# Performance work log

Measured on AMD Instinct MI355X. Metric: run time of the kernel, lower is better.

The kernel has to match this reference:

```python
import jax, jax.numpy as jnp
import numpy as np


def setup_inputs() -> dict:
    B, Lq, Lk, D, F, H = 2, 2048, 2048, 128, 128, 8
    key = jax.random.key(0)
    ks = jax.random.split(key, 8)
    X_Q = jax.random.normal(ks[0], (B, Lq, D), dtype=jnp.float32)
    X_K = jax.random.normal(ks[1], (B, Lk, D), dtype=jnp.float32)
    X_V = jax.random.normal(ks[2], (B, Lk, F), dtype=jnp.float32)
    mask = jax.random.randint(ks[3], (B, 1, Lq, Lk), 0, 2, dtype=jnp.int32)
    # xavier_normal for [H, D, D]: std = sqrt(2/(D+D))
    W_Q = jax.random.normal(ks[4], (H, D, D), dtype=jnp.float32) * np.sqrt(2.0 / (D + D))
    W_K = jax.random.normal(ks[5], (H, D, D), dtype=jnp.float32) * np.sqrt(2.0 / (D + D))
    W_V = jax.random.normal(ks[6], (H, F, F), dtype=jnp.float32) * np.sqrt(2.0 / (F + F))
    O = jax.random.normal(ks[7], (F * H, F), dtype=jnp.float32) * np.sqrt(2.0 / (F * H + F))
    return {"X_Q": X_Q, "X_K": X_K, "X_V": X_V, "mask": mask,
            "W_Q": W_Q, "W_K": W_K, "W_V": W_V, "O": O}


def reference(X_Q, X_K, X_V, mask, W_Q, W_K, W_V, O):
    B, Lq, D = X_Q.shape
    H = W_Q.shape[0]
    F = W_V.shape[1]
    # torch.einsum with repeated in-operand index ('hdd') takes the diagonal
    dq = jnp.diagonal(W_Q, axis1=1, axis2=2)  # [H, D]
    dk = jnp.diagonal(W_K, axis1=1, axis2=2)  # [H, D]
    dv = jnp.diagonal(W_V, axis1=1, axis2=2)  # [H, F]
    g = dq * dk                               # fused per-head QK diagonal scale [H, D]
    scale = 1.0 / jnp.sqrt(jnp.asarray(D, dtype=X_Q.dtype))
    scores = jnp.einsum('bqd,hd,bkd->bhqk', X_Q, g, X_K) * scale  # [B,H,Lq,Lk]
    scores = jnp.where(mask == 0, jnp.asarray(-jnp.inf, scores.dtype), scores)
    A = jax.nn.softmax(scores, axis=-1)
    # O_h = A @ (diag(dv_h) scaled V)
    Oh = jnp.einsum('bhqk,hf,bkf->bhqf', A, dv, X_V)  # [B,H,Lq,F]
    Oh = Oh.transpose(0, 2, 1, 3).reshape(B, Lq, H * F)
    return jnp.einsum('bqx,xf->bqf', Oh, O)
```

## Files before the change

### kernel.cpp

```cpp
#include <hip/hip_runtime.h>

typedef __bf16 bf16;
typedef __bf16 bf16x4 __attribute__((ext_vector_type(4)));
typedef __bf16 bf16x8 __attribute__((ext_vector_type(8)));
typedef float f32x4 __attribute__((ext_vector_type(4)));
typedef unsigned int u32;
typedef unsigned long long u64;

#define B_ 2
#define H_ 8
#define L_ 2048
#define D_ 128
#define F_ 128
#define QT 64
#define KT 64
#define NKT (L_ / KT)

#define WS_KB 0u
#define WS_VT (1u << 20)
#define WS_MB (2u << 20)

#define SMEM_BYTES 74752
#define SP_OFF 65536
#define SP_STRIDE 72
#define SOH_STRIDE 136
#define SO2_STRIDE 136

__device__ __forceinline__ void dma16(const void* g, void* l) {
    __builtin_amdgcn_global_load_lds(
        (const __attribute__((address_space(1))) u32*)g,
        (__attribute__((address_space(3))) u32*)l, 16, 0, 0);
}

__global__ __launch_bounds__(256) void prep_k(const float* __restrict__ XK, bf16* __restrict__ Kb) {
    int gid = blockIdx.x * 256 + threadIdx.x;
    int row = gid >> 4;
    int j   = gid & 15;
    const float* src = XK + (size_t)row * 128 + j * 8;
    float4 v0 = *(const float4*)src;
    float4 v1 = *(const float4*)(src + 4);
    bf16x8 w;
    w[0] = (bf16)v0.x; w[1] = (bf16)v0.y; w[2] = (bf16)v0.z; w[3] = (bf16)v0.w;
    w[4] = (bf16)v1.x; w[5] = (bf16)v1.y; w[6] = (bf16)v1.z; w[7] = (bf16)v1.w;
    int jp = j ^ (row & 15);
    *(bf16x8*)(Kb + (size_t)row * 128 + jp * 8) = w;
}

__global__ __launch_bounds__(256) void prep_v(const float* __restrict__ XV, bf16* __restrict__ Vtb) {
    __shared__ bf16 sT[64 * 128];
    int tile = blockIdx.x;
    int b = tile >> 5, kt = tile & 31;
    int k0 = kt * 64;
    int tid = threadIdx.x;
    int f4 = (tid & 31) * 4, kr = tid >> 5;
    #pragma unroll
    for (int i = 0; i < 8; ++i) {
        int k = kr + i * 8;
        float4 v = *(const float4*)(XV + (size_t)(b * L_ + k0 + k) * F_ + f4);
        bf16x4 w;
        w[0] = (bf16)v.x; w[1] = (bf16)v.y; w[2] = (bf16)v.z; w[3] = (bf16)v.w;
        *(bf16x4*)(sT + k * 128 + f4) = w;
    }
    __syncthreads();
    bf16* out = Vtb + (size_t)tile * (128 * 64);
    #pragma unroll
    for (int i = 0; i < 4; ++i) {
        int cid = tid * 4 + i;
        int f = cid >> 3, j = cid & 7;
        bf16x8 w;
        #pragma unroll
        for (int jj = 0; jj < 8; ++jj) w[jj] = sT[(j * 8 + jj) * 128 + f];
        *(bf16x8*)(out + f * 64 + (j ^ (f & 7)) * 8) = w;
    }
}

__global__ __launch_bounds__(256) void prep_mask(const int* __restrict__ mask, u64* __restrict__ bits) {
    size_t gid = (size_t)blockIdx.x * 256 + threadIdx.x;
    int m = mask[gid];
    u64 bal = __ballot(m != 0);
    if ((threadIdx.x & 63) == 0) bits[gid >> 6] = bal;
}

__global__ __launch_bounds__(256, 2)
void attn_fused_kernel(const float* __restrict__ XQ, const bf16* __restrict__ Kb,
                       const bf16* __restrict__ Vtb, const u64* __restrict__ bits,
                       const float* __restrict__ WQ, const float* __restrict__ WK,
                       const float* __restrict__ WV, const float* __restrict__ Om,
                       float* __restrict__ out)
{
    __shared__ __align__(16) char smem[SMEM_BYTES];
    __shared__ __align__(16) float g_s[128];

    bf16* sK0 = (bf16*)smem;
    bf16* sK1 = (bf16*)(smem + 16384);
    bf16* sV0 = (bf16*)(smem + 32768);
    bf16* sV1 = (bf16*)(smem + 49152);
    bf16* sP  = (bf16*)(smem + SP_OFF);
    bf16* sOh  = (bf16*)smem;
    bf16* sO2t = (bf16*)(smem + 17408);

    const int tid  = threadIdx.x;
    const int wave = tid >> 6;
    const int lane = tid & 63;
    const int c    = lane & 15;
    const int quad = lane >> 4;
    const int qt = blockIdx.x, h = blockIdx.y, b = blockIdx.z;
    const int q0 = qt * QT;
    const int fv  = tid & 127;
    const int grp = tid >> 7;

    if (tid < 128) {
        float wq = WQ[(h * D_ + tid) * D_ + tid];
        float wk = WK[(h * D_ + tid) * D_ + tid];
        g_s[tid] = wq * wk * 0.08838834764831845f;
    }
    __syncthreads();

    const char* gKbase = (const char*)Kb + (size_t)(b * L_) * 256;
    const char* gVbase = (const char*)Vtb + (size_t)(b * NKT) * 16384;

    #pragma unroll
    for (int i = 0; i < 4; ++i) dma16(gKbase + i * 4096 + tid * 16, (char*)sK0 + i * 4096 + tid * 16);
    #pragma unroll
    for (int i = 0; i < 4; ++i) dma16(gVbase + i * 4096 + tid * 16, (char*)sV0 + i * 4096 + tid * 16);

    bf16x8 qfrag[4];
    {
        const float* qrow = XQ + (size_t)(b * L_ + q0 + wave * 16 + c) * D_;
        #pragma unroll
        for (int kc = 0; kc < 4; ++kc) {
            int d0 = kc * 32 + quad * 8;
            float4 v0 = *(const float4*)(qrow + d0);
            float4 v1 = *(const float4*)(qrow + d0 + 4);
            float4 g0 = *(const float4*)(g_s + d0);
            float4 g1 = *(const float4*)(g_s + d0 + 4);
            bf16x8 w;
            w[0] = (bf16)(v0.x * g0.x); w[1] = (bf16)(v0.y * g0.y);
            w[2] = (bf16)(v0.z * g0.z); w[3] = (bf16)(v0.w * g0.w);
            w[4] = (bf16)(v1.x * g1.x); w[5] = (bf16)(v1.y * g1.y);
            w[6] = (bf16)(v1.z * g1.z); w[7] = (bf16)(v1.w * g1.w);
            qfrag[kc] = w;
        }
    }

    const int qrow0 = q0 + wave * 16 + quad * 4;
    const u64* mbase0 = bits + (size_t)(b * L_ + qrow0) * NKT;

    f32x4 oacc[8];
    #pragma unroll
    for (int i = 0; i < 8; ++i)
        #pragma unroll
        for (int r = 0; r < 4; ++r) oacc[i][r] = 0.f;
    float lsum[4] = {0.f, 0.f, 0.f, 0.f};

    #pragma unroll 2
    for (int kt = 0; kt < NKT; ++kt) {
        bf16* sK  = (kt & 1) ? sK1 : sK0;
        bf16* sV  = (kt & 1) ? sV1 : sV0;
        bf16* sKn = (kt & 1) ? sK0 : sK1;
        bf16* sVn = (kt & 1) ? sV0 : sV1;

        asm volatile("s_barrier" ::: "memory");

        u64 mb[4];
        const u64* mbase = mbase0 + kt;
        if (kt + 1 < NKT) {
            const char* gk = gKbase + (size_t)(kt + 1) * 16384;
            const char* gv = gVbase + (size_t)(kt + 1) * 16384;
            #pragma unroll
            for (int i = 0; i < 4; ++i) dma16(gk + i * 4096 + tid * 16, (char*)sKn + i * 4096 + tid * 16);
            #pragma unroll
            for (int i = 0; i < 4; ++i) dma16(gv + i * 4096 + tid * 16, (char*)sVn + i * 4096 + tid * 16);
            #pragma unroll
            for (int r = 0; r < 4; ++r) mb[r] = mbase[(size_t)r * NKT];
            asm volatile("s_waitcnt vmcnt(12)" ::: "memory");
        } else {
            #pragma unroll
            for (int r = 0; r < 4; ++r) mb[r] = mbase[(size_t)r * NKT];
            asm volatile("s_waitcnt vmcnt(4)" ::: "memory");
        }
        asm volatile("s_barrier" ::: "memory");

        f32x4 sacc[4];
        #pragma unroll
        for (int nt = 0; nt < 4; ++nt)
            #pragma unroll
            for (int r = 0; r < 4; ++r) sacc[nt][r] = 0.f;

        #pragma unroll
        for (int nt = 0; nt < 4; ++nt) {
            const bf16* krow = sK + (nt * 16 + c) * 128;
            #pragma unroll
            for (int kc = 0; kc < 4; ++kc) {
                bf16x8 bfrag = *(const bf16x8*)(krow + (((kc * 4 + quad) ^ c) * 8));
                sacc[nt] = __builtin_amdgcn_mfma_f32_16x16x32_bf16(qfrag[kc], bfrag, sacc[nt], 0, 0, 0);
            }
        }

        #pragma unroll
        for (int nt = 0; nt < 4; ++nt) {
            #pragma unroll
            for (int r = 0; r < 4; ++r) {
                float p = ((mb[r] >> (nt * 16 + c)) & 1ull) ? __expf(sacc[nt][r]) : 0.f;
                lsum[r] += p;
                sP[(wave * 16 + quad * 4 + r) * SP_STRIDE + nt * 16 + c] = (bf16)p;
            }
        }
        asm volatile("s_waitcnt lgkmcnt(0)" ::: "memory");

        bf16x8 pfrag[2];
        const bf16* prow = sP + (wave * 16 + c) * SP_STRIDE;
        #pragma unroll
        for (int kc = 0; kc < 2; ++kc)
            pfrag[kc] = *(const bf16x8*)(prow + kc * 32 + quad * 8);

        #pragma unroll
        for (int nt = 0; nt < 8; ++nt) {
            const bf16* vrow = sV + (nt * 16 + c) * 64;
            #pragma unroll
            for (int kc = 0; kc < 2; ++kc) {
                bf16x8 bfrag = *(const bf16x8*)(vrow + (((kc * 4 + quad) ^ (c & 7)) * 8));
                oacc[nt] = __builtin_amdgcn_mfma_f32_16x16x32_bf16(pfrag[kc], bfrag, oacc[nt], 0, 0, 0);
            }
        }
    }

    #pragma unroll
    for (int r = 0; r < 4; ++r) {
        float v = lsum[r];
        v += __shfl_xor(v, 1); v += __shfl_xor(v, 2);
        v += __shfl_xor(v, 4); v += __shfl_xor(v, 8);
        lsum[r] = 1.0f / v;
    }

    __syncthreads();

    if (tid < 128)
        g_s[tid] = WV[(h * F_ + tid) * F_ + tid];

    #pragma unroll
    for (int nt = 0; nt < 8; ++nt)
        #pragma unroll
        for (int r = 0; r < 4; ++r) {
            float v = oacc[nt][r] * lsum[r];
            sOh[(wave * 16 + quad * 4 + r) * SOH_STRIDE + nt * 16 + c] = (bf16)v;
        }
    __syncthreads();

    #pragma unroll
    for (int i = 0; i < 16; ++i) {
        int fp4 = grp * 64 + i * 4;
        bf16x4 w;
        #pragma unroll
        for (int j = 0; j < 4; ++j) {
            int x = fp4 + j;
            w[j] = (bf16)(Om[(h * F_ + x) * F_ + fv] * g_s[x]);
        }
        *(bf16x4*)(sO2t + fv * SO2_STRIDE + fp4) = w;
    }
    __syncthreads();

    bf16x8 afr[4];
    const bf16* ohrow = sOh + (wave * 16 + c) * SOH_STRIDE;
    #pragma unroll
    for (int kc = 0; kc < 4; ++kc)
        afr[kc] = *(const bf16x8*)(ohrow + kc * 32 + quad * 8);

    #pragma unroll
    for (int nt = 0; nt < 8; ++nt) {
        f32x4 pacc;
        #pragma unroll
        for (int r = 0; r < 4; ++r) pacc[r] = 0.f;
        const bf16* orow = sO2t + (nt * 16 + c) * SO2_STRIDE;
        #pragma unroll
        for (int kc = 0; kc < 4; ++kc) {
            bf16x8 bfrag = *(const bf16x8*)(orow + kc * 32 + quad * 8);
            pacc = __builtin_amdgcn_mfma_f32_16x16x32_bf16(afr[kc], bfrag, pacc, 0, 0, 0);
        }
        #pragma unroll
        for (int r = 0; r < 4; ++r) {
            int qg = q0 + wave * 16 + quad * 4 + r;
            atomicAdd(out + ((size_t)(b * L_ + qg) * F_ + nt * 16 + c), pacc[r]);
        }
    }
}

extern "C" void kernel_launch(void* const* d_in, const int* in_sizes, int n_in,
                              void* d_out, int out_size, void* d_ws, size_t ws_size,
                              hipStream_t stream) {
    const float* XQ   = (const float*)d_in[0];
    const float* XK   = (const float*)d_in[1];
    const float* XV   = (const float*)d_in[2];
    const int*   mask = (const int*)d_in[3];
    const float* WQ   = (const float*)d_in[4];
    const float* WK   = (const float*)d_in[5];
    const float* WV   = (const float*)d_in[6];
    const float* Om   = (const float*)d_in[7];
    float* out = (float*)d_out;

    char* ws = (char*)d_ws;
    bf16* Kb   = (bf16*)(ws + WS_KB);
    bf16* Vtb  = (bf16*)(ws + WS_VT);
    u64*  bits = (u64*)(ws + WS_MB);

    prep_k<<<256, 256, 0, stream>>>(XK, Kb);
    prep_v<<<B_ * NKT, 256, 0, stream>>>(XV, Vtb);
    prep_mask<<<(B_ * L_ * L_) / 256, 256, 0, stream>>>(mask, bits);
    hipMemsetAsync(out, 0, (size_t)out_size * sizeof(float), stream);

    dim3 grid(L_ / QT, H_, B_);
    attn_fused_kernel<<<grid, 256, 0, stream>>>(XQ, Kb, Vtb, bits, WQ, WK, WV, Om, out);
}
```

Measured before the change: 170.4 us.

## Split attention work by key rows per wave and fuse prep kernels

Merges the three preprocessing kernels (mask bit-packing, K conversion, V transpose) into one launch. The mask pass now has each wave handle four ballots, and V is transposed straight from global memory without a shared-memory stage. In the attention loop, each wave now computes the transposed score tile for its own 16 keys against all 64 queries. The PV product is then split as a 2x2 query-by-feature grid across the four waves, which needs an extra barrier per key tile and a cross-wave row-sum reduction through shared memory. Mask words are loaded per query row before the prefetch issue, and the added register pressure from qfrag[4][4] may hurt occupancy.

```diff
diff --git a/kernel.cpp b/kernel.cpp
--- a/kernel.cpp
+++ b/kernel.cpp
@@ -20,9 +20,10 @@
 #define WS_VT (1u << 20)
 #define WS_MB (2u << 20)
 
-#define SMEM_BYTES 74752
+#define SMEM_BYTES 75776
 #define SP_OFF 65536
 #define SP_STRIDE 72
+#define LWS_OFF 74752
 #define SOH_STRIDE 136
 #define SO2_STRIDE 136
 
@@ -32,53 +33,48 @@
         (__attribute__((address_space(3))) u32*)l, 16, 0, 0);
 }
 
-__global__ __launch_bounds__(256) void prep_k(const float* __restrict__ XK, bf16* __restrict__ Kb) {
-    int gid = blockIdx.x * 256 + threadIdx.x;
-    int row = gid >> 4;
-    int j   = gid & 15;
-    const float* src = XK + (size_t)row * 128 + j * 8;
-    float4 v0 = *(const float4*)src;
-    float4 v1 = *(const float4*)(src + 4);
-    bf16x8 w;
-    w[0] = (bf16)v0.x; w[1] = (bf16)v0.y; w[2] = (bf16)v0.z; w[3] = (bf16)v0.w;
-    w[4] = (bf16)v1.x; w[5] = (bf16)v1.y; w[6] = (bf16)v1.z; w[7] = (bf16)v1.w;
-    int jp = j ^ (row & 15);
-    *(bf16x8*)(Kb + (size_t)row * 128 + jp * 8) = w;
-}
-
-__global__ __launch_bounds__(256) void prep_v(const float* __restrict__ XV, bf16* __restrict__ Vtb) {
-    __shared__ bf16 sT[64 * 128];
-    int tile = blockIdx.x;
-    int b = tile >> 5, kt = tile & 31;
-    int k0 = kt * 64;
-    int tid = threadIdx.x;
-    int f4 = (tid & 31) * 4, kr = tid >> 5;
-    #pragma unroll
-    for (int i = 0; i < 8; ++i) {
-        int k = kr + i * 8;
-        float4 v = *(const float4*)(XV + (size_t)(b * L_ + k0 + k) * F_ + f4);
-        bf16x4 w;
-        w[0] = (bf16)v.x; w[1] = (bf16)v.y; w[2] = (bf16)v.z; w[3] = (bf16)v.w;
-        *(bf16x4*)(sT + k * 128 + f4) = w;
-    }
-    __syncthreads();
-    bf16* out = Vtb + (size_t)tile * (128 * 64);
-    #pragma unroll
-    for (int i = 0; i < 4; ++i) {
-        int cid = tid * 4 + i;
-        int f = cid >> 3, j = cid & 7;
+__global__ __launch_bounds__(256)
+void prep_all(const float* __restrict__ XK, const float* __restrict__ XV,
+              const int* __restrict__ mask, bf16* __restrict__ Kb,
+              bf16* __restrict__ Vtb, u64* __restrict__ bits)
+{
+    const int bid = blockIdx.x;
+    const int tid = threadIdx.x;
+    if (bid < 8192) {
+        int wv = bid * 4 + (tid >> 6);
+        int lane = tid & 63;
+        size_t base = (size_t)wv * 256;
+        #pragma unroll
+        for (int s = 0; s < 4; ++s) {
+            int m = mask[base + s * 64 + lane];
+            u64 bal = __ballot(m != 0);
+            if (lane == 0) bits[(size_t)wv * 4 + s] = bal;
+        }
+    } else if (bid < 8448) {
+        int gid = (bid - 8192) * 256 + tid;
+        int row = gid >> 4;
+        int j   = gid & 15;
+        const float* src = XK + (size_t)row * 128 + j * 8;
+        float4 v0 = *(const float4*)src;
+        float4 v1 = *(const float4*)(src + 4);
         bf16x8 w;
-        #pragma unroll
-        for (int jj = 0; jj < 8; ++jj) w[jj] = sT[(j * 8 + jj) * 128 + f];
-        *(bf16x8*)(out + f * 64 + (j ^ (f & 7)) * 8) = w;
-    }
-}
-
-__global__ __launch_bounds__(256) void prep_mask(const int* __restrict__ mask, u64* __restrict__ bits) {
-    size_t gid = (size_t)blockIdx.x * 256 + threadIdx.x;
-    int m = mask[gid];
-    u64 bal = __ballot(m != 0);
-    if ((threadIdx.x & 63) == 0) bits[gid >> 6] = bal;
+        w[0] = (bf16)v0.x; w[1] = (bf16)v0.y; w[2] = (bf16)v0.z; w[3] = (bf16)v0.w;
+        w[4] = (bf16)v1.x; w[5] = (bf16)v1.y; w[6] = (bf16)v1.z; w[7] = (bf16)v1.w;
+        int jp = j ^ (row & 15);
+        *(bf16x8*)(Kb + (size_t)row * 128 + jp * 8) = w;
+    } else {
+        int idx  = bid - 8448;
+        int tile = idx >> 2;
+        int fq   = idx & 3;
+        int f    = fq * 32 + (tid & 31);
+        int j    = tid >> 5;
+        int bb   = tile >> 5, kt = tile & 31;
+        const float* src = XV + ((size_t)(bb * L_ + kt * 64 + j * 8)) * F_ + f;
+        bf16x8 w;
+        #pragma unroll
+        for (int jj = 0; jj < 8; ++jj) w[jj] = (bf16)src[(size_t)jj * F_];
+        *(bf16x8*)(Vtb + (size_t)tile * 8192 + f * 64 + ((j ^ (f & 7)) * 8)) = w;
+    }
 }
 
 __global__ __launch_bounds__(256, 2)
@@ -96,6 +92,7 @@
     bf16* sV0 = (bf16*)(smem + 32768);
     bf16* sV1 = (bf16*)(smem + 49152);
     bf16* sP  = (bf16*)(smem + SP_OFF);
+    float* lws = (float*)(smem + LWS_OFF);
     bf16* sOh  = (bf16*)smem;
     bf16* sO2t = (bf16*)(smem + 17408);
 
@@ -106,6 +103,8 @@
     const int quad = lane >> 4;
     const int qt = blockIdx.x, h = blockIdx.y, b = blockIdx.z;
     const int q0 = qt * QT;
+    const int mh = wave >> 1;
+    const int fh = wave & 1;
     const int fv  = tid & 127;
     const int grp = tid >> 7;
 
@@ -124,9 +123,10 @@
     #pragma unroll
     for (int i = 0; i < 4; ++i) dma16(gVbase + i * 4096 + tid * 16, (char*)sV0 + i * 4096 + tid * 16);
 
-    bf16x8 qfrag[4];
-    {
-        const float* qrow = XQ + (size_t)(b * L_ + q0 + wave * 16 + c) * D_;
+    bf16x8 qfrag[4][4];
+    #pragma unroll
+    for (int mt = 0; mt < 4; ++mt) {
+        const float* qrow = XQ + (size_t)(b * L_ + q0 + mt * 16 + c) * D_;
         #pragma unroll
         for (int kc = 0; kc < 4; ++kc) {
             int d0 = kc * 32 + quad * 8;
@@ -139,19 +139,20 @@
             w[2] = (bf16)(v0.z * g0.z); w[3] = (bf16)(v0.w * g0.w);
             w[4] = (bf16)(v1.x * g1.x); w[5] = (bf16)(v1.y * g1.y);
             w[6] = (bf16)(v1.z * g1.z); w[7] = (bf16)(v1.w * g1.w);
-            qfrag[kc] = w;
-        }
-    }
-
-    const int qrow0 = q0 + wave * 16 + quad * 4;
-    const u64* mbase0 = bits + (size_t)(b * L_ + qrow0) * NKT;
-
-    f32x4 oacc[8];
-    #pragma unroll
-    for (int i = 0; i < 8; ++i)
-        #pragma unroll
-        for (int r = 0; r < 4; ++r) oacc[i][r] = 0.f;
+            qfrag[mt][kc] = w;
+        }
+    }
+
+    f32x4 oacc[2][4];
+    #pragma unroll
+    for (int mi = 0; mi < 2; ++mi)
+        #pragma unroll
+        for (int fi = 0; fi < 4; ++fi)
+            #pragma unroll
+            for (int r = 0; r < 4; ++r) oacc[mi][fi][r] = 0.f;
     float lsum[4] = {0.f, 0.f, 0.f, 0.f};
+
+    const int shift = wave * 16 + quad * 4;
 
     #pragma unroll 2
     for (int kt = 0; kt < NKT; ++kt) {
@@ -163,7 +164,10 @@
         asm volatile("s_barrier" ::: "memory");
 
         u64 mb[4];
-        const u64* mbase = mbase0 + kt;
+        #pragma unroll
+        for (int mt = 0; mt < 4; ++mt)
+            mb[mt] = bits[(size_t)(b * L_ + q0 + mt * 16 + c) * NKT + kt];
+
         if (kt + 1 < NKT) {
             const char* gk = gKbase + (size_t)(kt + 1) * 16384;
             const char* gv = gVbase + (size_t)(kt + 1) * 16384;
@@ -171,80 +175,88 @@
             for (int i = 0; i < 4; ++i) dma16(gk + i * 4096 + tid * 16, (char*)sKn + i * 4096 + tid * 16);
             #pragma unroll
             for (int i = 0; i < 4; ++i) dma16(gv + i * 4096 + tid * 16, (char*)sVn + i * 4096 + tid * 16);
-            #pragma unroll
-            for (int r = 0; r < 4; ++r) mb[r] = mbase[(size_t)r * NKT];
             asm volatile("s_waitcnt vmcnt(12)" ::: "memory");
         } else {
-            #pragma unroll
-            for (int r = 0; r < 4; ++r) mb[r] = mbase[(size_t)r * NKT];
             asm volatile("s_waitcnt vmcnt(4)" ::: "memory");
         }
         asm volatile("s_barrier" ::: "memory");
 
-        f32x4 sacc[4];
-        #pragma unroll
-        for (int nt = 0; nt < 4; ++nt)
-            #pragma unroll
-            for (int r = 0; r < 4; ++r) sacc[nt][r] = 0.f;
-
-        #pragma unroll
-        for (int nt = 0; nt < 4; ++nt) {
-            const bf16* krow = sK + (nt * 16 + c) * 128;
-            #pragma unroll
-            for (int kc = 0; kc < 4; ++kc) {
-                bf16x8 bfrag = *(const bf16x8*)(krow + (((kc * 4 + quad) ^ c) * 8));
-                sacc[nt] = __builtin_amdgcn_mfma_f32_16x16x32_bf16(qfrag[kc], bfrag, sacc[nt], 0, 0, 0);
+        f32x4 tacc[4];
+        #pragma unroll
+        for (int mt = 0; mt < 4; ++mt)
+            #pragma unroll
+            for (int r = 0; r < 4; ++r) tacc[mt][r] = 0.f;
+
+        const bf16* krow = sK + (wave * 16 + c) * 128;
+        #pragma unroll
+        for (int kc = 0; kc < 4; ++kc) {
+            bf16x8 kfrag = *(const bf16x8*)(krow + (((kc * 4 + quad) ^ c) * 8));
+            #pragma unroll
+            for (int mt = 0; mt < 4; ++mt)
+                tacc[mt] = __builtin_amdgcn_mfma_f32_16x16x32_bf16(kfrag, qfrag[mt][kc], tacc[mt], 0, 0, 0);
+        }
+
+        #pragma unroll
+        for (int mt = 0; mt < 4; ++mt) {
+            bf16x4 pw;
+            #pragma unroll
+            for (int r = 0; r < 4; ++r) {
+                float p = ((mb[mt] >> (shift + r)) & 1ull) ? __expf(tacc[mt][r]) : 0.f;
+                lsum[mt] += p;
+                pw[r] = (bf16)p;
             }
-        }
-
-        #pragma unroll
-        for (int nt = 0; nt < 4; ++nt) {
-            #pragma unroll
-            for (int r = 0; r < 4; ++r) {
-                float p = ((mb[r] >> (nt * 16 + c)) & 1ull) ? __expf(sacc[nt][r]) : 0.f;
-                lsum[r] += p;
-                sP[(wave * 16 + quad * 4 + r) * SP_STRIDE + nt * 16 + c] = (bf16)p;
+            *(bf16x4*)(sP + (mt * 16 + c) * SP_STRIDE + shift) = pw;
+        }
+        asm volatile("s_waitcnt lgkmcnt(0)" ::: "memory");
+        asm volatile("s_barrier" ::: "memory");
+
+        #pragma unroll
+        for (int kc = 0; kc < 2; ++kc) {
+            bf16x8 pfrag[2];
+            #pragma unroll
+            for (int mi = 0; mi < 2; ++mi)
+                pfrag[mi] = *(const bf16x8*)(sP + ((2 * mh + mi) * 16 + c) * SP_STRIDE + kc * 32 + quad * 8);
+            #pragma unroll
+            for (int fi = 0; fi < 4; ++fi) {
+                const bf16* vrow = sV + ((fh * 4 + fi) * 16 + c) * 64;
+                bf16x8 vfrag = *(const bf16x8*)(vrow + (((kc * 4 + quad) ^ (c & 7)) * 8));
+                #pragma unroll
+                for (int mi = 0; mi < 2; ++mi)
+                    oacc[mi][fi] = __builtin_amdgcn_mfma_f32_16x16x32_bf16(pfrag[mi], vfrag, oacc[mi][fi], 0, 0, 0);
             }
         }
-        asm volatile("s_waitcnt lgkmcnt(0)" ::: "memory");
-
-        bf16x8 pfrag[2];
-        const bf16* prow = sP + (wave * 16 + c) * SP_STRIDE;
-        #pragma unroll
-        for (int kc = 0; kc < 2; ++kc)
-            pfrag[kc] = *(const bf16x8*)(prow + kc * 32 + quad * 8);
-
-        #pragma unroll
-        for (int nt = 0; nt < 8; ++nt) {
-            const bf16* vrow = sV + (nt * 16 + c) * 64;
-            #pragma unroll
-            for (int kc = 0; kc < 2; ++kc) {
-                bf16x8 bfrag = *(const bf16x8*)(vrow + (((kc * 4 + quad) ^ (c & 7)) * 8));
-                oacc[nt] = __builtin_amdgcn_mfma_f32_16x16x32_bf16(pfrag[kc], bfrag, oacc[nt], 0, 0, 0);
-            }
-        }
-    }
-
-    #pragma unroll
-    for (int r = 0; r < 4; ++r) {
-        float v = lsum[r];
-        v += __shfl_xor(v, 1); v += __shfl_xor(v, 2);
-        v += __shfl_xor(v, 4); v += __shfl_xor(v, 8);
-        lsum[r] = 1.0f / v;
-    }
-
+    }
+
+    #pragma unroll
+    for (int mt = 0; mt < 4; ++mt) {
+        float v = lsum[mt];
+        v += __shfl_xor(v, 16); v += __shfl_xor(v, 32);
+        if (lane < 16) lws[wave * 64 + mt * 16 + lane] = v;
+    }
     __syncthreads();
 
     if (tid < 128)
         g_s[tid] = WV[(h * F_ + tid) * F_ + tid];
 
-    #pragma unroll
-    for (int nt = 0; nt < 8; ++nt)
+    float linv[2][4];
+    #pragma unroll
+    for (int mi = 0; mi < 2; ++mi)
         #pragma unroll
         for (int r = 0; r < 4; ++r) {
-            float v = oacc[nt][r] * lsum[r];
-            sOh[(wave * 16 + quad * 4 + r) * SOH_STRIDE + nt * 16 + c] = (bf16)v;
-        }
+            int q_local = (2 * mh + mi) * 16 + quad * 4 + r;
+            float s = lws[q_local] + lws[64 + q_local] + lws[128 + q_local] + lws[192 + q_local];
+            linv[mi][r] = 1.0f / s;
+        }
+    #pragma unroll
+    for (int mi = 0; mi < 2; ++mi)
+        #pragma unroll
+        for (int fi = 0; fi < 4; ++fi)
+            #pragma unroll
+            for (int r = 0; r < 4; ++r) {
+                int q_local = (2 * mh + mi) * 16 + quad * 4 + r;
+                int f_col   = (fh * 4 + fi) * 16 + c;
+                sOh[q_local * SOH_STRIDE + f_col] = (bf16)(oacc[mi][fi][r] * linv[mi][r]);
+            }
     __syncthreads();
 
     #pragma unroll
@@ -303,9 +315,7 @@
     bf16* Vtb  = (bf16*)(ws + WS_VT);
     u64*  bits = (u64*)(ws + WS_MB);
 
-    prep_k<<<256, 256, 0, stream>>>(XK, Kb);
-    prep_v<<<B_ * NKT, 256, 0, stream>>>(XV, Vtb);
-    prep_mask<<<(B_ * L_ * L_) / 256, 256, 0, stream>>>(mask, bits);
+    prep_all<<<8704, 256, 0, stream>>>(XK, XV, mask, Kb, Vtb, bits);
     hipMemsetAsync(out, 0, (size_t)out_size * sizeof(float), stream);
 
     dim3 grid(L_ / QT, H_, B_);
```

Result: faster. 166.3 us (-2.5%).
